# Kernel optimization log

Hardware: AMD Instinct MI355X
Metric: run time of the kernel (lower is better)

## Reference

```python
import jax, jax.numpy as jnp
import numpy as np

VOCAB, S, D, H, DH, L, W1S, DFF = 50265, 4096, 768, 12, 64, 2, 256, 3072


def layer_norm(x, g, b, eps=1e-5):
    m = jnp.mean(x, axis=-1, keepdims=True)
    v = jnp.mean((x - m) ** 2, axis=-1, keepdims=True)
    return (x - m) * jax.lax.rsqrt(v + eps) * g + b


def sliding_global_attn(q, k, v, att, w=W1S):
    # q,k,v: [B,H,S,Dh]; att: [B,S] float (1 real / 0 pad). Longformer-style
    # sliding window (one-sided w) + global attention on token 0.
    B, nh, S_, Dh = q.shape
    nc = S_ // w
    q = q * (Dh ** -0.5)
    k_pad = jnp.pad(k, ((0, 0), (0, 0), (w, w), (0, 0)))
    v_pad = jnp.pad(v, ((0, 0), (0, 0), (w, w), (0, 0)))
    idx = jnp.arange(nc)[:, None] * w + jnp.arange(3 * w)[None, :]  # [nc,3w] into padded axis
    k_band = k_pad[:, :, idx]  # [B,H,nc,3w,Dh]
    v_band = v_pad[:, :, idx]
    qc = q.reshape(B, nh, nc, w, Dh)
    s_loc = jnp.einsum('bhcqd,bhckd->bhcqk', qc, k_band)  # [B,H,nc,w,3w]
    rel = jnp.arange(3 * w)[None, :] - jnp.arange(w)[:, None]  # [w,3w]
    band_ok = (rel >= 0) & (rel <= 2 * w)
    key_abs = idx - w  # [nc,3w] absolute key positions
    in_seq = (key_abs >= 0) & (key_abs < S_) & (key_abs != 0)  # token 0 handled by global column
    key_real = att[:, jnp.clip(key_abs, 0, S_ - 1)] > 0  # [B,nc,3w]
    valid = band_ok[None, None, None] & in_seq[None, None, :, None, :] & key_real[:, None, :, None, :]
    s_loc = jnp.where(valid, s_loc, -1e9)
    s_g = jnp.einsum('bhcqd,bhd->bhcq', qc, k[:, :, 0])  # global key column
    p = jax.nn.softmax(jnp.concatenate([s_g[..., None], s_loc], axis=-1), axis=-1)
    out = (jnp.einsum('bhcq,bhd->bhcqd', p[..., 0], v[:, :, 0])
           + jnp.einsum('bhcqk,bhckd->bhcqd', p[..., 1:], v_band)).reshape(B, nh, S_, Dh)
    # global token 0 attends to everything
    s0 = jnp.where(att[:, None, :] > 0, jnp.einsum('bhd,bhsd->bhs', q[:, :, 0], k), -1e9)
    out0 = jnp.einsum('bhs,bhsd->bhd', jax.nn.softmax(s0, axis=-1), v)
    return out.at[:, :, 0].set(out0)


def setup_inputs() -> dict:
    key = jax.random.key(0)
    ks = jax.random.split(key, 16)
    sc = 0.02
    inp = {
        'input_ids': jax.random.randint(ks[0], (2, S), 0, VOCAB, dtype=jnp.int64)
        if jax.config.jax_enable_x64 else jax.random.randint(ks[0], (2, S), 0, VOCAB, dtype=jnp.int32),
        'attention_mask': jnp.ones((2, S), dtype=jnp.int32),
        'word_emb': sc * jax.random.normal(ks[1], (VOCAB, D), jnp.float32),
        'pos_emb': sc * jax.random.normal(ks[2], (S, D), jnp.float32),
        'emb_ln_g': jnp.ones((D,), jnp.float32), 'emb_ln_b': jnp.zeros((D,), jnp.float32),
        'Wq': sc * jax.random.normal(ks[3], (L, D, D), jnp.float32), 'bq': jnp.zeros((L, D), jnp.float32),
        'Wk': sc * jax.random.normal(ks[4], (L, D, D), jnp.float32), 'bk': jnp.zeros((L, D), jnp.float32),
        'Wv': sc * jax.random.normal(ks[5], (L, D, D), jnp.float32), 'bv': jnp.zeros((L, D), jnp.float32),
        'Wo': sc * jax.random.normal(ks[6], (L, D, D), jnp.float32), 'bo': jnp.zeros((L, D), jnp.float32),
        'ln1_g': jnp.ones((L, D), jnp.float32), 'ln1_b': jnp.zeros((L, D), jnp.float32),
        'Wf1': sc * jax.random.normal(ks[7], (L, D, DFF), jnp.float32), 'bf1': jnp.zeros((L, DFF), jnp.float32),
        'Wf2': sc * jax.random.normal(ks[8], (L, DFF, D), jnp.float32), 'bf2': jnp.zeros((L, D), jnp.float32),
        'ln2_g': jnp.ones((L, D), jnp.float32), 'ln2_b': jnp.zeros((L, D), jnp.float32),
        'Wh1': sc * jax.random.normal(ks[9], (D, 256), jnp.float32), 'bh1': jnp.zeros((256,), jnp.float32),
        'Wh2': sc * jax.random.normal(ks[10], (256, 14), jnp.float32), 'bh2': jnp.zeros((14,), jnp.float32),
    }
    return inp


def reference(input_ids, attention_mask, word_emb, pos_emb, emb_ln_g, emb_ln_b,
              Wq, bq, Wk, bk, Wv, bv, Wo, bo, ln1_g, ln1_b,
              Wf1, bf1, Wf2, bf2, ln2_g, ln2_b, Wh1, bh1, Wh2, bh2):
    B, S_ = input_ids.shape
    att = attention_mask.astype(jnp.float32)
    x = word_emb[input_ids] + pos_emb[None, :S_, :]
    x = layer_norm(x, emb_ln_g, emb_ln_b)
    for l in range(L):
        def heads(w, b):
            return (x @ w + b).reshape(B, S_, H, DH).transpose(0, 2, 1, 3)
        q = heads(Wq[l], bq[l]); k = heads(Wk[l], bk[l]); v = heads(Wv[l], bv[l])
        a = sliding_global_attn(q, k, v, att)
        a = a.transpose(0, 2, 1, 3).reshape(B, S_, D) @ Wo[l] + bo[l]
        x = layer_norm(x + a, ln1_g[l], ln1_b[l])
        f = jax.nn.gelu(x @ Wf1[l] + bf1[l]) @ Wf2[l] + bf2[l]
        x = layer_norm(x + f, ln2_g[l], ln2_b[l])
    # masked mean pool
    m = att[..., None]
    pooled = jnp.sum(x * m, axis=1) / jnp.clip(jnp.sum(m, axis=1), 1e-9)
    h = jax.nn.relu(pooled @ Wh1 + bh1)
    return jax.nn.sigmoid(h @ Wh2 + bh2) * 4.0
```

## Files before the change

### kernel.cpp

```cpp
#include <hip/hip_runtime.h>
#include <hip/hip_bf16.h>
#include <math.h>

#define S_LEN 4096
#define D_MODEL 768
#define NHEAD 12
#define DH 64
#define NLAYER 2
#define DFF 3072
#define BATCH 2
#define QSTR 2304

typedef __attribute__((ext_vector_type(8))) __bf16 bf16x8;
typedef __attribute__((ext_vector_type(4))) float f32x4;
typedef __attribute__((ext_vector_type(16))) float f32x16;

__device__ __forceinline__ unsigned short f2bf_bits(float f) {
  unsigned int u = __float_as_uint(f);
  unsigned int r = (u + 0x7fffu + ((u >> 16) & 1u)) >> 16;
  return (unsigned short)r;
}

__device__ __forceinline__ float bf2f(unsigned short u) {
  return __uint_as_float(((unsigned int)u) << 16);
}

__device__ __forceinline__ unsigned int cvtpk_bf16(float lo, float hi) {
  unsigned int d;
  asm("v_cvt_pk_bf16_f32 %0, %1, %2" : "=v"(d) : "v"(lo), "v"(hi));
  return d;
}

__device__ __forceinline__ float gelu_fast(float x) {
  float u = 0.7978845608028654f * (x + 0.044715f * x * x * x);
  float t2 = fminf(fmaxf(2.f * u, -18.f), 18.f);
  float e = __expf(t2);
  return 0.5f * x * (1.f + (e - 1.f) / (e + 1.f));
}

#define ASYNC_COPY16(gsrc, ldst)                                       \
  __builtin_amdgcn_global_load_lds(                                    \
      (const __attribute__((address_space(1))) void*)(gsrc),           \
      (__attribute__((address_space(3))) void*)(ldst), 16, 0, 0)

#define MFMA_BF16(a, b, c) __builtin_amdgcn_mfma_f32_16x16x32_bf16(a, b, c, 0, 0, 0)
#define MFMA32_BF16(a, b, c) __builtin_amdgcn_mfma_f32_32x32x16_bf16(a, b, c, 0, 0, 0)

__device__ __forceinline__ float blk_sum256(float v, float* lds) {
#pragma unroll
  for (int off = 32; off > 0; off >>= 1) v += __shfl_down(v, off, 64);
  __syncthreads();
  if ((threadIdx.x & 63) == 0) lds[threadIdx.x >> 6] = v;
  __syncthreads();
  return lds[0] + lds[1] + lds[2] + lds[3];
}

__global__ __launch_bounds__(256) void wconv_kernel(
    const float* __restrict__ Wq, const float* __restrict__ Wk,
    const float* __restrict__ Wv, const float* __restrict__ Wo,
    const float* __restrict__ Wf1, const float* __restrict__ Wf2,
    unsigned short* __restrict__ Wbf) {
  int id = blockIdx.x;
  const float* src;
  unsigned short* dst;
  int K, N, t;
  if (id < 4608) {
    int m = id / 576;
    t = id % 576;
    int layer = m >> 2, which = m & 3;
    const float* s = (which == 0) ? Wq : (which == 1) ? Wk : (which == 2) ? Wv : Wo;
    src = s + (size_t)layer * 589824;
    dst = Wbf + (size_t)layer * 7077888 + (size_t)which * 589824;
    K = 768; N = 768;
  } else if (id < 9216) {
    int j = id - 4608;
    int layer = j / 2304;
    t = j % 2304;
    src = Wf1 + (size_t)layer * 2359296;
    dst = Wbf + (size_t)layer * 7077888 + 2359296;
    K = 768; N = 3072;
  } else {
    int j = id - 9216;
    int layer = j / 2304;
    t = j % 2304;
    src = Wf2 + (size_t)layer * 2359296;
    dst = Wbf + (size_t)layer * 7077888 + 4718592;
    K = 3072; N = 768;
  }
  int tiles_n = N >> 5;
  int tk = t / tiles_n, tn = t % tiles_n;
  __shared__ float tile[32][33];
  int c = threadIdx.x & 31, r0 = threadIdx.x >> 5;
#pragma unroll
  for (int p = 0; p < 4; ++p) {
    int r = r0 + p * 8;
    tile[r][c] = src[(size_t)(tk * 32 + r) * N + tn * 32 + c];
  }
  __syncthreads();
#pragma unroll
  for (int p = 0; p < 4; ++p) {
    int r = r0 + p * 8;
    dst[(size_t)(tn * 32 + r) * K + tk * 32 + c] = f2bf_bits(tile[c][r]);
  }
}

__global__ __launch_bounds__(256) void embed_ln_kernel(
    const int* __restrict__ ids, const float* __restrict__ wemb,
    const float* __restrict__ pemb, const float* __restrict__ g,
    const float* __restrict__ b, unsigned short* __restrict__ Xb) {
  int row = blockIdx.x;
  int s = row % S_LEN;
  int id = ids[row];
  const float* we = wemb + (size_t)id * D_MODEL;
  const float* pe = pemb + (size_t)s * D_MODEL;
  int t = threadIdx.x;
  __shared__ float lds[4];
  float v0 = we[t] + pe[t];
  float v1 = we[t + 256] + pe[t + 256];
  float v2 = we[t + 512] + pe[t + 512];
  float mean = blk_sum256(v0 + v1 + v2, lds) * (1.f / 768.f);
  float d0 = v0 - mean, d1 = v1 - mean, d2 = v2 - mean;
  float var = blk_sum256(d0 * d0 + d1 * d1 + d2 * d2, lds) * (1.f / 768.f);
  float rs = rsqrtf(var + 1e-5f);
  unsigned short* xb = Xb + (size_t)row * D_MODEL;
  xb[t]       = f2bf_bits(d0 * rs * g[t] + b[t]);
  xb[t + 256] = f2bf_bits(d1 * rs * g[t + 256] + b[t + 256]);
  xb[t + 512] = f2bf_bits(d2 * rs * g[t + 512] + b[t + 512]);
}

__global__ __launch_bounds__(256) void ln_kernel(
    const float* __restrict__ T, const float* __restrict__ g,
    const float* __restrict__ b, unsigned short* __restrict__ Xb) {
  int row = blockIdx.x;
  const float* tp = T + (size_t)row * D_MODEL;
  int t = threadIdx.x;
  __shared__ float lds[4];
  float v0 = tp[t], v1 = tp[t + 256], v2 = tp[t + 512];
  float mean = blk_sum256(v0 + v1 + v2, lds) * (1.f / 768.f);
  float d0 = v0 - mean, d1 = v1 - mean, d2 = v2 - mean;
  float var = blk_sum256(d0 * d0 + d1 * d1 + d2 * d2, lds) * (1.f / 768.f);
  float rs = rsqrtf(var + 1e-5f);
  unsigned short* xb = Xb + (size_t)row * D_MODEL;
  xb[t]       = f2bf_bits(d0 * rs * g[t] + b[t]);
  xb[t + 256] = f2bf_bits(d1 * rs * g[t + 256] + b[t + 256]);
  xb[t + 512] = f2bf_bits(d2 * rs * g[t + 512] + b[t + 512]);
}

template <int MODE>
__global__ __launch_bounds__(256) void gemm32(
    const unsigned short* __restrict__ A, const unsigned short* __restrict__ Bt,
    const float* __restrict__ bias0, const float* __restrict__ bias1,
    const float* __restrict__ bias2, const unsigned short* __restrict__ ResBf,
    void* __restrict__ Cout, int M, int N, int K) {
  __shared__ unsigned short Abuf[3][128 * 32];
  __shared__ unsigned short Bbuf[3][128 * 32];
  const int tid = threadIdx.x;
  const int lane = tid & 63, w = tid >> 6;
  const int wm = w >> 1, wn = w & 1;
  const int l31 = lane & 31, l5 = lane >> 5;

  const int nbx = gridDim.x;
  const int nwg = nbx * gridDim.y;
  const int orig = blockIdx.y * nbx + blockIdx.x;
  const int wgid = (orig & 7) * (nwg >> 3) + (orig >> 3);
  const int m0 = (wgid / nbx) * 128, n0 = (wgid % nbx) * 128;

  f32x16 acc[2][2];
#pragma unroll
  for (int i = 0; i < 2; ++i)
#pragma unroll
    for (int j = 0; j < 2; ++j)
#pragma unroll
      for (int r = 0; r < 16; ++r) acc[i][j][r] = 0.f;

  const int s0 = w * 64 + lane, s1 = s0 + 256;
  const int r0 = s0 >> 2, c0 = (s0 & 3) ^ ((r0 >> 1) & 3);
  const int r1 = s1 >> 2, c1 = (s1 & 3) ^ ((r1 >> 1) & 3);
  const unsigned short* gA0 = A + (size_t)(m0 + r0) * K + c0 * 8;
  const unsigned short* gA1 = A + (size_t)(m0 + r1) * K + c1 * 8;
  const unsigned short* gB0 = Bt + (size_t)(n0 + r0) * K + c0 * 8;
  const unsigned short* gB1 = Bt + (size_t)(n0 + r1) * K + c1 * 8;
  const int dA0 = (w * 64) * 8, dA1 = (256 + w * 64) * 8;

  int aoff[2][2], boff[2][2];
#pragma unroll
  for (int mt = 0; mt < 2; ++mt) {
    int ra = wm * 64 + mt * 32 + l31;
    int rb = wn * 64 + mt * 32 + l31;
    int key_a = (ra >> 1) & 3, key_b = (rb >> 1) & 3;
#pragma unroll
    for (int ks = 0; ks < 2; ++ks) {
      aoff[mt][ks] = ra * 32 + ((((ks << 1) | l5) ^ key_a) << 3);
      boff[mt][ks] = rb * 32 + ((((ks << 1) | l5) ^ key_b) << 3);
    }
  }

#define STAGE(bsel)                                                       \
  {                                                                       \
    ASYNC_COPY16(gA0, &Abuf[bsel][dA0]);                                  \
    ASYNC_COPY16(gA1, &Abuf[bsel][dA1]);                                  \
    ASYNC_COPY16(gB0, &Bbuf[bsel][dA0]);                                  \
    ASYNC_COPY16(gB1, &Bbuf[bsel][dA1]);                                  \
    gA0 += 32; gA1 += 32; gB0 += 32; gB1 += 32;                           \
  }

  const int nk = K >> 5;
  STAGE(0);
  if (nk > 1) STAGE(1);
  asm volatile("s_waitcnt vmcnt(4)" ::: "memory");
  __builtin_amdgcn_s_barrier();
  __builtin_amdgcn_sched_barrier(0);

  int cur = 0;
  for (int kt = 0; kt < nk; ++kt) {
    if (kt + 2 < nk) {
      int nxt = cur + 2;
      if (nxt >= 3) nxt -= 3;
      STAGE(nxt);
    }
    bf16x8 av[2][2], bv[2][2];
#pragma unroll
    for (int mt = 0; mt < 2; ++mt)
#pragma unroll
      for (int ks = 0; ks < 2; ++ks) {
        av[mt][ks] = *(const bf16x8*)(&Abuf[cur][aoff[mt][ks]]);
        bv[mt][ks] = *(const bf16x8*)(&Bbuf[cur][boff[mt][ks]]);
      }
#pragma unroll
    for (int mt = 0; mt < 2; ++mt)
#pragma unroll
      for (int nt = 0; nt < 2; ++nt)
#pragma unroll
        for (int ks = 0; ks < 2; ++ks)
          acc[mt][nt] = MFMA32_BF16(av[mt][ks], bv[nt][ks], acc[mt][nt]);
    if (kt + 1 < nk) {
      if (kt + 2 < nk)
        asm volatile("s_waitcnt vmcnt(4)" ::: "memory");
      else
        asm volatile("s_waitcnt vmcnt(0)" ::: "memory");
      __builtin_amdgcn_s_barrier();
      __builtin_amdgcn_sched_barrier(0);
    }
    cur = (cur == 2) ? 0 : cur + 1;
  }
#undef STAGE

#pragma unroll
  for (int mt = 0; mt < 2; ++mt) {
#pragma unroll
    for (int nt = 0; nt < 2; ++nt) {
      int gc = n0 + wn * 64 + nt * 32 + l31;
      float bsv;
      if (MODE == 4)
        bsv = (gc < 768) ? bias0[gc] : (gc < 1536) ? bias1[gc - 768] : bias2[gc - 1536];
      else
        bsv = bias0[gc];
#pragma unroll
      for (int reg = 0; reg < 16; ++reg) {
        int gr = m0 + wm * 64 + mt * 32 + (reg & 3) + 8 * (reg >> 2) + 4 * l5;
        float v = acc[mt][nt][reg] + bsv;
        if (MODE == 1) v = gelu_fast(v);
        if (MODE == 4 && gc < 768) v *= 0.125f;
        if (MODE == 2) {
          v += bf2f(ResBf[(size_t)gr * 768 + gc]);
          ((float*)Cout)[(size_t)gr * N + gc] = v;
        } else {
          ((unsigned short*)Cout)[(size_t)gr * N + gc] = f2bf_bits(v);
        }
      }
    }
  }
}

__global__ __launch_bounds__(256) void vtrans_kernel(
    const unsigned short* __restrict__ Vsrc, unsigned short* __restrict__ Vt) {
  int kb = blockIdx.x, h = blockIdx.y, b = blockIdx.z;
  int k0 = kb * 64;
  const size_t bs = (size_t)b * S_LEN;
  const size_t bh = (size_t)(b * NHEAD + h);
  __shared__ unsigned short tile[64][72];
  int tid = threadIdx.x;
#pragma unroll
  for (int p = 0; p < 2; ++p) {
    int idx = p * 256 + tid;
    int key = idx >> 3, ch = idx & 7;
    bf16x8 v = *(const bf16x8*)(Vsrc + (bs + k0 + key) * QSTR + h * DH + ch * 8);
    *(bf16x8*)&tile[key][ch * 8] = v;
  }
  __syncthreads();
#pragma unroll
  for (int p = 0; p < 2; ++p) {
    int idx = p * 256 + tid;
    int d = idx >> 3, kc = idx & 7;
    unsigned int w0 = tile[kc * 8 + 0][d] | ((unsigned int)tile[kc * 8 + 1][d] << 16);
    unsigned int w1 = tile[kc * 8 + 2][d] | ((unsigned int)tile[kc * 8 + 3][d] << 16);
    unsigned int w2 = tile[kc * 8 + 4][d] | ((unsigned int)tile[kc * 8 + 5][d] << 16);
    unsigned int w3 = tile[kc * 8 + 6][d] | ((unsigned int)tile[kc * 8 + 7][d] << 16);
    uint4 out = make_uint4(w0, w1, w2, w3);
    *(uint4*)(Vt + (bh * 64 + d) * S_LEN + k0 + kc * 8) = out;
  }
}

__global__ __launch_bounds__(512) void band_attn_kernel(
    const unsigned short* __restrict__ Qg, const unsigned short* __restrict__ Kgb,
    const unsigned short* __restrict__ Vgb, const unsigned short* __restrict__ Vt,
    const int* __restrict__ att, unsigned short* __restrict__ Aout) {
  const int c = blockIdx.x, h = blockIdx.y, b = blockIdx.z;
  const int tid = threadIdx.x;
  const int lane = tid & 63, wq = tid >> 6;
  const int g = lane >> 4, cl = lane & 15;
  const size_t bs = (size_t)b * S_LEN;
  const size_t bh = (size_t)(b * NHEAD + h);

  __shared__ __align__(16) char smem[33280];

  if (c == 32) {
    float* sc = (float*)smem;
    float* q0 = sc + S_LEN;
    float* red = q0 + 64;
    float* part = red + 8;
    if (tid < 64) q0[tid] = bf2f(Qg[bs * QSTR + h * DH + tid]);
    __syncthreads();
    float lmax = -1e30f;
    for (int s = tid; s < S_LEN; s += 512) {
      const unsigned short* kp = Kgb + (bs + s) * QSTR + h * DH;
      float acc = 0.f;
#pragma unroll
      for (int cc = 0; cc < 8; ++cc) {
        uint4 u = *(const uint4*)(kp + cc * 8);
        const unsigned int* uu = (const unsigned int*)&u;
#pragma unroll
        for (int w2 = 0; w2 < 4; ++w2) {
          unsigned int x = uu[w2];
          acc += q0[cc * 8 + w2 * 2] * __uint_as_float(x << 16);
          acc += q0[cc * 8 + w2 * 2 + 1] * __uint_as_float(x & 0xffff0000u);
        }
      }
      acc = (att[b * S_LEN + s] > 0) ? acc : -1e9f;
      sc[s] = acc;
      lmax = fmaxf(lmax, acc);
    }
#pragma unroll
    for (int off = 32; off > 0; off >>= 1) lmax = fmaxf(lmax, __shfl_down(lmax, off, 64));
    __syncthreads();
    if (lane == 0) red[wq] = lmax;
    __syncthreads();
    float M = red[0];
#pragma unroll
    for (int i = 1; i < 8; ++i) M = fmaxf(M, red[i]);
    float lsum = 0.f;
    for (int s = tid; s < S_LEN; s += 512) {
      float p = __expf(sc[s] - M);
      sc[s] = p;
      lsum += p;
    }
#pragma unroll
    for (int off = 32; off > 0; off >>= 1) lsum += __shfl_down(lsum, off, 64);
    __syncthreads();
    if (lane == 0) red[wq] = lsum;
    __syncthreads();
    float L = red[0];
#pragma unroll
    for (int i = 1; i < 8; ++i) L += red[i];
    int d = tid & 63, chunk = tid >> 6;
    float acc2 = 0.f;
    for (int s = chunk * 512; s < (chunk + 1) * 512; ++s)
      acc2 += sc[s] * bf2f(Vgb[(bs + s) * QSTR + h * DH + d]);
    part[chunk * 64 + d] = acc2;
    __syncthreads();
    if (tid < 64) {
      float v = 0.f;
#pragma unroll
      for (int i = 0; i < 8; ++i) v += part[i * 64 + tid];
      Aout[bs * D_MODEL + h * DH + tid] = f2bf_bits(v / L);
    }
    return;
  }

  unsigned short* Klds = (unsigned short*)smem;
  unsigned short* Vlds = Klds + 2 * 4096;
  float* kmask = (float*)(Vlds + 2 * 4096);

  const int Q0 = c * 128;

  bf16x8 qf[2];
#pragma unroll
  for (int ks = 0; ks < 2; ++ks)
    qf[ks] = *(const bf16x8*)(Qg + (bs + Q0 + wq * 16 + cl) * QSTR +
                              h * DH + ks * 32 + g * 8);

  float mrun, lrun;
  f32x4 oacc[4];
  {
    float sg = 0.f;
#pragma unroll
    for (int ks = 0; ks < 2; ++ks) {
      bf16x8 k0 = *(const bf16x8*)(Kgb + bs * QSTR + h * DH + ks * 32 + g * 8);
#pragma unroll
      for (int j = 0; j < 8; ++j) sg += (float)qf[ks][j] * (float)k0[j];
    }
    sg += __shfl_xor(sg, 16, 64);
    sg += __shfl_xor(sg, 32, 64);
    mrun = sg;
    lrun = 1.f;
#pragma unroll
    for (int dt = 0; dt < 4; ++dt) {
      float v0d = bf2f(Vgb[bs * QSTR + h * DH + dt * 16 + cl]);
      oacc[dt] = (f32x4){v0d, v0d, v0d, v0d};
    }
  }

  const int jwlo = wq * 16, jwhi = wq * 16 + 543;
  const int tlo = (Q0 < 256) ? ((256 - Q0) >> 6) : 0;
  int thi = (S_LEN - Q0 + 256) >> 6;
  if (thi > 10) thi = 10;

  const int skey = tid >> 3, sch = tid & 7;
  const int swz = (sch ^ (skey & 7)) * 8;

  auto LOADT = [&](int t, bf16x8& kr, bf16x8& vr) {
    int kb0 = Q0 - 256 + t * 64;
    kr = *(const bf16x8*)(Kgb + (bs + kb0 + skey) * QSTR + h * DH + sch * 8);
    vr = *(const bf16x8*)(Vt + (bh * 64 + skey) * S_LEN + kb0 + sch * 8);
  };
  auto WRITET = [&](int p, int t, bf16x8 kr, bf16x8 vr) {
    *(bf16x8*)(Klds + p * 4096 + skey * 64 + swz) = kr;
    *(bf16x8*)(Vlds + p * 4096 + skey * 64 + swz) = vr;
    if (tid < 64) {
      int ka = Q0 - 256 + t * 64 + tid;
      kmask[p * 64 + tid] = (ka >= 1 && att[b * S_LEN + ka] > 0) ? 0.f : -1e9f;
    }
  };

  auto COMPUTE = [&](int p, int t) {
    if (t * 64 + 63 < jwlo || t * 64 > jwhi) return;
    f32x4 accs[4];
#pragma unroll
    for (int kt = 0; kt < 4; ++kt) accs[kt] = (f32x4){0.f, 0.f, 0.f, 0.f};
#pragma unroll
    for (int ks = 0; ks < 2; ++ks) {
      bf16x8 kf[4];
#pragma unroll
      for (int kt = 0; kt < 4; ++kt) {
        int key = kt * 16 + cl;
        kf[kt] = *(const bf16x8*)(Klds + p * 4096 + key * 64 +
                                  (((ks * 4 + g) ^ (key & 7)) * 8));
      }
#pragma unroll
      for (int kt = 0; kt < 4; ++kt)
        accs[kt] = MFMA_BF16(kf[kt], qf[ks], accs[kt]);
    }

    int iq = wq * 16 + cl;
    int relbase = t * 64 - iq;
    float pvv[4][4];
    float tmax = -1e30f;
#pragma unroll
    for (int kt = 0; kt < 4; ++kt)
#pragma unroll
      for (int r = 0; r < 4; ++r) {
        int key = kt * 16 + g * 4 + r;
        int rel = relbase + key;
        float x = accs[kt][r] + kmask[p * 64 + key];
        x = (rel >= 0 && rel <= 512) ? x : -1e9f;
        pvv[kt][r] = x;
        tmax = fmaxf(tmax, x);
      }
    tmax = fmaxf(tmax, __shfl_xor(tmax, 16, 64));
    tmax = fmaxf(tmax, __shfl_xor(tmax, 32, 64));
    float mnew = fmaxf(mrun, tmax);
    float scale = __expf(mrun - mnew);
    mrun = mnew;
    float psum = 0.f;
#pragma unroll
    for (int kt = 0; kt < 4; ++kt)
#pragma unroll
      for (int r = 0; r < 4; ++r) {
        float pp = __expf(pvv[kt][r] - mnew);
        pvv[kt][r] = pp;
        psum += pp;
      }
    psum += __shfl_xor(psum, 16, 64);
    psum += __shfl_xor(psum, 32, 64);
    lrun = lrun * scale + psum;
    float scr[4];
#pragma unroll
    for (int r = 0; r < 4; ++r) scr[r] = __shfl(scale, g * 4 + r, 64);
#pragma unroll
    for (int dt = 0; dt < 4; ++dt) {
      oacc[dt][0] *= scr[0];
      oacc[dt][1] *= scr[1];
      oacc[dt][2] *= scr[2];
      oacc[dt][3] *= scr[3];
    }
#pragma unroll
    for (int ks = 0; ks < 2; ++ks) {
      unsigned int E0D0 = cvtpk_bf16(pvv[ks * 2][0], pvv[ks * 2][1]);
      unsigned int E0D1 = cvtpk_bf16(pvv[ks * 2][2], pvv[ks * 2][3]);
      unsigned int E1D0 = cvtpk_bf16(pvv[ks * 2 + 1][0], pvv[ks * 2 + 1][1]);
      unsigned int E1D1 = cvtpk_bf16(pvv[ks * 2 + 1][2], pvv[ks * 2 + 1][3]);
      int src0 = ((lane >> 4) & 1) * 32 + cl;
      int src1 = src0 + 16;
      unsigned int a0 = (unsigned int)__shfl((int)E0D0, src0, 64);
      unsigned int a1 = (unsigned int)__shfl((int)E0D1, src0, 64);
      unsigned int a2 = (unsigned int)__shfl((int)E0D0, src1, 64);
      unsigned int a3 = (unsigned int)__shfl((int)E0D1, src1, 64);
      unsigned int b0 = (unsigned int)__shfl((int)E1D0, src0, 64);
      unsigned int b1 = (unsigned int)__shfl((int)E1D1, src0, 64);
      unsigned int b2 = (unsigned int)__shfl((int)E1D0, src1, 64);
      unsigned int b3 = (unsigned int)__shfl((int)E1D1, src1, 64);
      bool hi = lane >= 32;
      union { unsigned int u[4]; bf16x8 v; } af;
      af.u[0] = hi ? b0 : a0;
      af.u[1] = hi ? b1 : a1;
      af.u[2] = hi ? b2 : a2;
      af.u[3] = hi ? b3 : a3;
#pragma unroll
      for (int dt = 0; dt < 4; ++dt) {
        int d = dt * 16 + cl;
        bf16x8 vf = *(const bf16x8*)(Vlds + p * 4096 + d * 64 +
                                     (((ks * 4 + g) ^ (d & 7)) * 8));
        oacc[dt] = MFMA_BF16(af.v, vf, oacc[dt]);
      }
    }
  };

  bf16x8 kA, vA, kB, vB;
  LOADT(tlo, kA, vA);
  for (int t = tlo; t < thi; t += 2) {
    __builtin_amdgcn_s_barrier();
    WRITET(0, t, kA, vA);
    if (t + 1 < thi) LOADT(t + 1, kB, vB);
    asm volatile("s_waitcnt lgkmcnt(0)" ::: "memory");
    __builtin_amdgcn_s_barrier();
    __builtin_amdgcn_sched_barrier(0);
    COMPUTE(0, t);
    if (t + 1 >= thi) break;
    __builtin_amdgcn_s_barrier();
    WRITET(1, t + 1, kB, vB);
    if (t + 2 < thi) LOADT(t + 2, kA, vA);
    asm volatile("s_waitcnt lgkmcnt(0)" ::: "memory");
    __builtin_amdgcn_s_barrier();
    __builtin_amdgcn_sched_barrier(0);
    COMPUTE(1, t + 1);
  }

  float lr[4];
#pragma unroll
  for (int r = 0; r < 4; ++r) lr[r] = 1.f / __shfl(lrun, g * 4 + r, 64);
#pragma unroll
  for (int dt = 0; dt < 4; ++dt)
#pragma unroll
    for (int r = 0; r < 4; ++r) {
      int row = Q0 + wq * 16 + g * 4 + r;
      if (row != 0)
        Aout[(bs + row) * D_MODEL + h * DH + dt * 16 + cl] =
            f2bf_bits(oacc[dt][r] * lr[r]);
    }
}

__global__ __launch_bounds__(256) void pool1_kernel(
    const unsigned short* __restrict__ Xb, const int* __restrict__ att,
    float* __restrict__ ppart) {
  int sb = blockIdx.x, b = blockIdx.y, t = threadIdx.x;
  float a0 = 0.f, a1 = 0.f, a2 = 0.f;
  for (int s = sb * 256; s < sb * 256 + 256; ++s) {
    float a = (float)att[b * S_LEN + s];
    const unsigned short* xp = Xb + ((size_t)b * S_LEN + s) * D_MODEL;
    a0 += bf2f(xp[t]) * a; a1 += bf2f(xp[t + 256]) * a; a2 += bf2f(xp[t + 512]) * a;
  }
  float* pp = ppart + ((size_t)b * 16 + sb) * D_MODEL;
  pp[t] = a0; pp[t + 256] = a1; pp[t + 512] = a2;
}

__global__ __launch_bounds__(256) void pool2_kernel(
    const float* __restrict__ ppart, const int* __restrict__ att,
    float* __restrict__ pooled) {
  int b = blockIdx.x, t = threadIdx.x;
  float a0 = 0.f, a1 = 0.f, a2 = 0.f;
  for (int sb = 0; sb < 16; ++sb) {
    const float* pp = ppart + ((size_t)b * 16 + sb) * D_MODEL;
    a0 += pp[t]; a1 += pp[t + 256]; a2 += pp[t + 512];
  }
  float cnt = 0.f;
  for (int s = 0; s < S_LEN; ++s) cnt += (float)att[b * S_LEN + s];
  cnt = fmaxf(cnt, 1e-9f);
  pooled[b * D_MODEL + t]       = a0 / cnt;
  pooled[b * D_MODEL + t + 256] = a1 / cnt;
  pooled[b * D_MODEL + t + 512] = a2 / cnt;
}

__global__ __launch_bounds__(256) void head_kernel(
    const float* __restrict__ pooled, const float* __restrict__ Wh1,
    const float* __restrict__ bh1, const float* __restrict__ Wh2,
    const float* __restrict__ bh2, float* __restrict__ out) {
  __shared__ float hbuf[2][256];
  int t = threadIdx.x;
  for (int b = 0; b < 2; ++b) {
    float acc = bh1[t];
    for (int d = 0; d < D_MODEL; ++d) acc += pooled[b * D_MODEL + d] * Wh1[d * 256 + t];
    hbuf[b][t] = fmaxf(acc, 0.f);
  }
  __syncthreads();
  if (t < 28) {
    int b = t / 14, j = t % 14;
    float acc = bh2[j];
    for (int i = 0; i < 256; ++i) acc += hbuf[b][i] * Wh2[i * 14 + j];
    out[t] = 4.f / (1.f + __expf(-acc));
  }
}

extern "C" void kernel_launch(void* const* d_in, const int* in_sizes, int n_in,
                              void* d_out, int out_size, void* d_ws,
                              size_t ws_size, hipStream_t stream) {
  const int* ids    = (const int*)d_in[0];
  const int* att    = (const int*)d_in[1];
  const float* wemb = (const float*)d_in[2];
  const float* pemb = (const float*)d_in[3];
  const float* elng = (const float*)d_in[4];
  const float* elnb = (const float*)d_in[5];
  const float* Wq   = (const float*)d_in[6];
  const float* bq   = (const float*)d_in[7];
  const float* Wk   = (const float*)d_in[8];
  const float* bk   = (const float*)d_in[9];
  const float* Wv   = (const float*)d_in[10];
  const float* bv   = (const float*)d_in[11];
  const float* Wo   = (const float*)d_in[12];
  const float* bo   = (const float*)d_in[13];
  const float* ln1g = (const float*)d_in[14];
  const float* ln1b = (const float*)d_in[15];
  const float* Wf1  = (const float*)d_in[16];
  const float* bf1  = (const float*)d_in[17];
  const float* Wf2  = (const float*)d_in[18];
  const float* bf2  = (const float*)d_in[19];
  const float* ln2g = (const float*)d_in[20];
  const float* ln2b = (const float*)d_in[21];
  const float* Wh1  = (const float*)d_in[22];
  const float* bh1  = (const float*)d_in[23];
  const float* Wh2  = (const float*)d_in[24];
  const float* bh2  = (const float*)d_in[25];

  const int M = BATCH * S_LEN;
  float* ws = (float*)d_ws;
  float* T = ws;
  unsigned short* QKV  = (unsigned short*)(ws + 6291456);
  unsigned short* Vt   = (unsigned short*)(ws + 11010048);
  unsigned short* Abbf = (unsigned short*)(ws + 12582912);
  unsigned short* Xbf  = (unsigned short*)(ws + 15728640);
  unsigned short* FFbf = (unsigned short*)(ws + 18874368);
  unsigned short* Wbf  = (unsigned short*)(ws + 31457280);
  float* pooled = ws + 38535168;
  float* ppart  = ws + 38536704;

  wconv_kernel<<<13824, 256, 0, stream>>>(Wq, Wk, Wv, Wo, Wf1, Wf2, Wbf);
  embed_ln_kernel<<<M, 256, 0, stream>>>(ids, wemb, pemb, elng, elnb, Xbf);

  for (int l = 0; l < NLAYER; ++l) {
    const unsigned short* wqkv = Wbf + (size_t)l * 7077888;
    const unsigned short* wot  = wqkv + 1769472;
    const unsigned short* wf1t = wqkv + 2359296;
    const unsigned short* wf2t = wqkv + 4718592;

    gemm32<4><<<dim3(18, 64), 256, 0, stream>>>(
        Xbf, wqkv, bq + l * D_MODEL, bk + l * D_MODEL, bv + l * D_MODEL,
        nullptr, QKV, M, QSTR, 768);

    vtrans_kernel<<<dim3(64, NHEAD, BATCH), 256, 0, stream>>>(QKV + 1536, Vt);
    band_attn_kernel<<<dim3(33, NHEAD, BATCH), 512, 0, stream>>>(
        QKV, QKV + 768, QKV + 1536, Vt, att, Abbf);

    gemm32<2><<<dim3(6, 64), 256, 0, stream>>>(
        Abbf, wot, bo + l * D_MODEL, nullptr, nullptr, Xbf, T, M, 768, 768);
    ln_kernel<<<M, 256, 0, stream>>>(T, ln1g + l * D_MODEL, ln1b + l * D_MODEL, Xbf);

    gemm32<1><<<dim3(24, 64), 256, 0, stream>>>(
        Xbf, wf1t, bf1 + l * DFF, nullptr, nullptr, nullptr, FFbf, M, DFF, 768);
    gemm32<2><<<dim3(6, 64), 256, 0, stream>>>(
        FFbf, wf2t, bf2 + l * D_MODEL, nullptr, nullptr, Xbf, T, M, 768, DFF);
    ln_kernel<<<M, 256, 0, stream>>>(T, ln2g + l * D_MODEL, ln2b + l * D_MODEL, Xbf);
  }

  pool1_kernel<<<dim3(16, BATCH), 256, 0, stream>>>(Xbf, att, ppart);
  pool2_kernel<<<BATCH, 256, 0, stream>>>(ppart, att, pooled);
  head_kernel<<<1, 256, 0, stream>>>(pooled, Wh1, bh1, Wh2, bh2, (float*)d_out);
}
```

Measured before the change: 998.3 us.

## Restructure band attention: 256-query tiles, async triple-buffered K/V, XCD-aware block mapping

```diff
diff --git a/kernel.cpp b/kernel.cpp
--- a/kernel.cpp
+++ b/kernel.cpp
@@ -305,16 +305,17 @@
     const unsigned short* __restrict__ Qg, const unsigned short* __restrict__ Kgb,
     const unsigned short* __restrict__ Vgb, const unsigned short* __restrict__ Vt,
     const int* __restrict__ att, unsigned short* __restrict__ Aout) {
-  const int c = blockIdx.x, h = blockIdx.y, b = blockIdx.z;
+  const int bid = blockIdx.x;
   const int tid = threadIdx.x;
   const int lane = tid & 63, wq = tid >> 6;
   const int g = lane >> 4, cl = lane & 15;
-  const size_t bs = (size_t)b * S_LEN;
-  const size_t bh = (size_t)(b * NHEAD + h);
-
-  __shared__ __align__(16) char smem[33280];
-
-  if (c == 32) {
+
+  __shared__ __align__(16) char smem[52224];
+
+  if (bid >= 384) {
+    int g2 = bid - 384;
+    int h = g2 % NHEAD, b = g2 / NHEAD;
+    const size_t bs = (size_t)b * S_LEN;
     float* sc = (float*)smem;
     float* q0 = sc + S_LEN;
     float* red = q0 + 64;
@@ -377,66 +378,83 @@
     return;
   }
 
+  const int xcd = bid & 7, within = bid >> 3;
+  const int flat = xcd * 48 + within;
+  const int c = flat & 15;
+  const int hb = flat >> 4;
+  const int h = hb % NHEAD, b = hb / NHEAD;
+  const size_t bs = (size_t)b * S_LEN;
+  const size_t bh = (size_t)(b * NHEAD + h);
+
   unsigned short* Klds = (unsigned short*)smem;
-  unsigned short* Vlds = Klds + 2 * 4096;
-  float* kmask = (float*)(Vlds + 2 * 4096);
-
-  const int Q0 = c * 128;
-
-  bf16x8 qf[2];
-#pragma unroll
-  for (int ks = 0; ks < 2; ++ks)
-    qf[ks] = *(const bf16x8*)(Qg + (bs + Q0 + wq * 16 + cl) * QSTR +
-                              h * DH + ks * 32 + g * 8);
-
-  float mrun, lrun;
-  f32x4 oacc[4];
-  {
+  unsigned short* Vlds = Klds + 3 * 4096;
+  float* kmaskAll = (float*)(Vlds + 3 * 4096);
+
+  const int Q0 = c * 256;
+
+  bf16x8 qf[2][2];
+#pragma unroll
+  for (int qt = 0; qt < 2; ++qt)
+#pragma unroll
+    for (int ks = 0; ks < 2; ++ks)
+      qf[qt][ks] = *(const bf16x8*)(Qg + (bs + Q0 + wq * 32 + qt * 16 + cl) * QSTR +
+                                    h * DH + ks * 32 + g * 8);
+
+  float mrun[2], lrun[2];
+  f32x4 oacc[2][4];
+#pragma unroll
+  for (int qt = 0; qt < 2; ++qt) {
     float sg = 0.f;
 #pragma unroll
     for (int ks = 0; ks < 2; ++ks) {
       bf16x8 k0 = *(const bf16x8*)(Kgb + bs * QSTR + h * DH + ks * 32 + g * 8);
 #pragma unroll
-      for (int j = 0; j < 8; ++j) sg += (float)qf[ks][j] * (float)k0[j];
+      for (int j = 0; j < 8; ++j) sg += (float)qf[qt][ks][j] * (float)k0[j];
     }
     sg += __shfl_xor(sg, 16, 64);
     sg += __shfl_xor(sg, 32, 64);
-    mrun = sg;
-    lrun = 1.f;
-#pragma unroll
-    for (int dt = 0; dt < 4; ++dt) {
-      float v0d = bf2f(Vgb[bs * QSTR + h * DH + dt * 16 + cl]);
-      oacc[dt] = (f32x4){v0d, v0d, v0d, v0d};
-    }
-  }
-
-  const int jwlo = wq * 16, jwhi = wq * 16 + 543;
-  const int tlo = (Q0 < 256) ? ((256 - Q0) >> 6) : 0;
-  int thi = (S_LEN - Q0 + 256) >> 6;
-  if (thi > 10) thi = 10;
+    mrun[qt] = sg;
+    lrun[qt] = 1.f;
+  }
+#pragma unroll
+  for (int dt = 0; dt < 4; ++dt) {
+    float v0d = bf2f(Vgb[bs * QSTR + h * DH + dt * 16 + cl]);
+    f32x4 vv = {v0d, v0d, v0d, v0d};
+    oacc[0][dt] = vv;
+    oacc[1][dt] = vv;
+  }
+  for (int i = tid; i < 768; i += 512) {
+    int ka = Q0 - 256 + i;
+    kmaskAll[i] = (ka >= 1 && ka < S_LEN && att[b * S_LEN + ka] > 0) ? 0.f : -1e9f;
+  }
+  __syncthreads();
+
+  const int jlo = wq * 32, jhi = wq * 32 + 543;
+  const int tlo = (Q0 < 256) ? 4 : 0;
+  int thi = (S_LEN + 256 - Q0) >> 6;
+  if (thi > 12) thi = 12;
 
   const int skey = tid >> 3, sch = tid & 7;
-  const int swz = (sch ^ (skey & 7)) * 8;
-
-  auto LOADT = [&](int t, bf16x8& kr, bf16x8& vr) {
+  const int srcswzK = (sch ^ (skey & 7)) * 8;
+
+  auto STAGE_T = [&](int t) {
+    int p = t % 3;
     int kb0 = Q0 - 256 + t * 64;
-    kr = *(const bf16x8*)(Kgb + (bs + kb0 + skey) * QSTR + h * DH + sch * 8);
-    vr = *(const bf16x8*)(Vt + (bh * 64 + skey) * S_LEN + kb0 + sch * 8);
+    const unsigned short* srcK = Kgb + (bs + kb0 + skey) * QSTR + h * DH + srcswzK;
+    const unsigned short* srcV = Vt + (bh * 64 + skey) * S_LEN + kb0 + srcswzK;
+    ASYNC_COPY16(srcK, Klds + p * 4096 + wq * 512);
+    ASYNC_COPY16(srcV, Vlds + p * 4096 + wq * 512);
   };
-  auto WRITET = [&](int p, int t, bf16x8 kr, bf16x8 vr) {
-    *(bf16x8*)(Klds + p * 4096 + skey * 64 + swz) = kr;
-    *(bf16x8*)(Vlds + p * 4096 + skey * 64 + swz) = vr;
-    if (tid < 64) {
-      int ka = Q0 - 256 + t * 64 + tid;
-      kmask[p * 64 + tid] = (ka >= 1 && att[b * S_LEN + ka] > 0) ? 0.f : -1e9f;
-    }
-  };
-
-  auto COMPUTE = [&](int p, int t) {
-    if (t * 64 + 63 < jwlo || t * 64 > jwhi) return;
-    f32x4 accs[4];
-#pragma unroll
-    for (int kt = 0; kt < 4; ++kt) accs[kt] = (f32x4){0.f, 0.f, 0.f, 0.f};
+
+  auto COMPUTE = [&](int t) {
+    if (t * 64 + 63 < jlo || t * 64 > jhi) return;
+    int p = t % 3;
+    f32x4 accs[4][2];
+#pragma unroll
+    for (int kt = 0; kt < 4; ++kt) {
+      accs[kt][0] = (f32x4){0.f, 0.f, 0.f, 0.f};
+      accs[kt][1] = (f32x4){0.f, 0.f, 0.f, 0.f};
+    }
 #pragma unroll
     for (int ks = 0; ks < 2; ++ks) {
       bf16x8 kf[4];
@@ -447,116 +465,117 @@
                                   (((ks * 4 + g) ^ (key & 7)) * 8));
       }
 #pragma unroll
+      for (int kt = 0; kt < 4; ++kt) {
+        accs[kt][0] = MFMA_BF16(kf[kt], qf[0][ks], accs[kt][0]);
+        accs[kt][1] = MFMA_BF16(kf[kt], qf[1][ks], accs[kt][1]);
+      }
+    }
+
+#pragma unroll
+    for (int qt = 0; qt < 2; ++qt) {
+      int iq = wq * 32 + qt * 16 + cl;
+      int relbase = t * 64 - iq;
+      float pvv[4][4];
+      float tmax = -1e30f;
+#pragma unroll
       for (int kt = 0; kt < 4; ++kt)
-        accs[kt] = MFMA_BF16(kf[kt], qf[ks], accs[kt]);
-    }
-
-    int iq = wq * 16 + cl;
-    int relbase = t * 64 - iq;
-    float pvv[4][4];
-    float tmax = -1e30f;
-#pragma unroll
-    for (int kt = 0; kt < 4; ++kt)
-#pragma unroll
-      for (int r = 0; r < 4; ++r) {
-        int key = kt * 16 + g * 4 + r;
-        int rel = relbase + key;
-        float x = accs[kt][r] + kmask[p * 64 + key];
-        x = (rel >= 0 && rel <= 512) ? x : -1e9f;
-        pvv[kt][r] = x;
-        tmax = fmaxf(tmax, x);
+#pragma unroll
+        for (int r = 0; r < 4; ++r) {
+          int key = kt * 16 + g * 4 + r;
+          int rel = relbase + key;
+          float x = accs[kt][qt][r] + kmaskAll[t * 64 + key];
+          x = (rel >= 0 && rel <= 512) ? x : -1e9f;
+          pvv[kt][r] = x;
+          tmax = fmaxf(tmax, x);
+        }
+      tmax = fmaxf(tmax, __shfl_xor(tmax, 16, 64));
+      tmax = fmaxf(tmax, __shfl_xor(tmax, 32, 64));
+      float mnew = fmaxf(mrun[qt], tmax);
+      float scale = __expf(mrun[qt] - mnew);
+      mrun[qt] = mnew;
+      float psum = 0.f;
+#pragma unroll
+      for (int kt = 0; kt < 4; ++kt)
+#pragma unroll
+        for (int r = 0; r < 4; ++r) {
+          float pp = __expf(pvv[kt][r] - mnew);
+          pvv[kt][r] = pp;
+          psum += pp;
+        }
+      psum += __shfl_xor(psum, 16, 64);
+      psum += __shfl_xor(psum, 32, 64);
+      lrun[qt] = lrun[qt] * scale + psum;
+      float scr[4];
+#pragma unroll
+      for (int r = 0; r < 4; ++r) scr[r] = __shfl(scale, g * 4 + r, 64);
+#pragma unroll
+      for (int dt = 0; dt < 4; ++dt) {
+        oacc[qt][dt][0] *= scr[0];
+        oacc[qt][dt][1] *= scr[1];
+        oacc[qt][dt][2] *= scr[2];
+        oacc[qt][dt][3] *= scr[3];
       }
-    tmax = fmaxf(tmax, __shfl_xor(tmax, 16, 64));
-    tmax = fmaxf(tmax, __shfl_xor(tmax, 32, 64));
-    float mnew = fmaxf(mrun, tmax);
-    float scale = __expf(mrun - mnew);
-    mrun = mnew;
-    float psum = 0.f;
-#pragma unroll
-    for (int kt = 0; kt < 4; ++kt)
-#pragma unroll
-      for (int r = 0; r < 4; ++r) {
-        float pp = __expf(pvv[kt][r] - mnew);
-        pvv[kt][r] = pp;
-        psum += pp;
+#pragma unroll
+      for (int ks = 0; ks < 2; ++ks) {
+        unsigned int E0D0 = cvtpk_bf16(pvv[ks * 2][0], pvv[ks * 2][1]);
+        unsigned int E0D1 = cvtpk_bf16(pvv[ks * 2][2], pvv[ks * 2][3]);
+        unsigned int E1D0 = cvtpk_bf16(pvv[ks * 2 + 1][0], pvv[ks * 2 + 1][1]);
+        unsigned int E1D1 = cvtpk_bf16(pvv[ks * 2 + 1][2], pvv[ks * 2 + 1][3]);
+        int src0 = ((lane >> 4) & 1) * 32 + cl;
+        int src1 = src0 + 16;
+        unsigned int a0 = (unsigned int)__shfl((int)E0D0, src0, 64);
+        unsigned int a1 = (unsigned int)__shfl((int)E0D1, src0, 64);
+        unsigned int a2 = (unsigned int)__shfl((int)E0D0, src1, 64);
+        unsigned int a3 = (unsigned int)__shfl((int)E0D1, src1, 64);
+        unsigned int b0 = (unsigned int)__shfl((int)E1D0, src0, 64);
+        unsigned int b1 = (unsigned int)__shfl((int)E1D1, src0, 64);
+        unsigned int b2 = (unsigned int)__shfl((int)E1D0, src1, 64);
+        unsigned int b3 = (unsigned int)__shfl((int)E1D1, src1, 64);
+        bool hi = lane >= 32;
+        union { unsigned int u[4]; bf16x8 v; } af;
+        af.u[0] = hi ? b0 : a0;
+        af.u[1] = hi ? b1 : a1;
+        af.u[2] = hi ? b2 : a2;
+        af.u[3] = hi ? b3 : a3;
+#pragma unroll
+        for (int dt = 0; dt < 4; ++dt) {
+          int d = dt * 16 + cl;
+          bf16x8 vf = *(const bf16x8*)(Vlds + p * 4096 + d * 64 +
+                                       (((ks * 4 + g) ^ (d & 7)) * 8));
+          oacc[qt][dt] = MFMA_BF16(af.v, vf, oacc[qt][dt]);
+        }
       }
-    psum += __shfl_xor(psum, 16, 64);
-    psum += __shfl_xor(psum, 32, 64);
-    lrun = lrun * scale + psum;
-    float scr[4];
-#pragma unroll
-    for (int r = 0; r < 4; ++r) scr[r] = __shfl(scale, g * 4 + r, 64);
-#pragma unroll
-    for (int dt = 0; dt < 4; ++dt) {
-      oacc[dt][0] *= scr[0];
-      oacc[dt][1] *= scr[1];
-      oacc[dt][2] *= scr[2];
-      oacc[dt][3] *= scr[3];
-    }
-#pragma unroll
-    for (int ks = 0; ks < 2; ++ks) {
-      unsigned int E0D0 = cvtpk_bf16(pvv[ks * 2][0], pvv[ks * 2][1]);
-      unsigned int E0D1 = cvtpk_bf16(pvv[ks * 2][2], pvv[ks * 2][3]);
-      unsigned int E1D0 = cvtpk_bf16(pvv[ks * 2 + 1][0], pvv[ks * 2 + 1][1]);
-      unsigned int E1D1 = cvtpk_bf16(pvv[ks * 2 + 1][2], pvv[ks * 2 + 1][3]);
-      int src0 = ((lane >> 4) & 1) * 32 + cl;
-      int src1 = src0 + 16;
-      unsigned int a0 = (unsigned int)__shfl((int)E0D0, src0, 64);
-      unsigned int a1 = (unsigned int)__shfl((int)E0D1, src0, 64);
-      unsigned int a2 = (unsigned int)__shfl((int)E0D0, src1, 64);
-      unsigned int a3 = (unsigned int)__shfl((int)E0D1, src1, 64);
-      unsigned int b0 = (unsigned int)__shfl((int)E1D0, src0, 64);
-      unsigned int b1 = (unsigned int)__shfl((int)E1D1, src0, 64);
-      unsigned int b2 = (unsigned int)__shfl((int)E1D0, src1, 64);
-      unsigned int b3 = (unsigned int)__shfl((int)E1D1, src1, 64);
-      bool hi = lane >= 32;
-      union { unsigned int u[4]; bf16x8 v; } af;
-      af.u[0] = hi ? b0 : a0;
-      af.u[1] = hi ? b1 : a1;
-      af.u[2] = hi ? b2 : a2;
-      af.u[3] = hi ? b3 : a3;
-#pragma unroll
-      for (int dt = 0; dt < 4; ++dt) {
-        int d = dt * 16 + cl;
-        bf16x8 vf = *(const bf16x8*)(Vlds + p * 4096 + d * 64 +
-                                     (((ks * 4 + g) ^ (d & 7)) * 8));
-        oacc[dt] = MFMA_BF16(af.v, vf, oacc[dt]);
-      }
     }
   };
 
-  bf16x8 kA, vA, kB, vB;
-  LOADT(tlo, kA, vA);
-  for (int t = tlo; t < thi; t += 2) {
-    __builtin_amdgcn_s_barrier();
-    WRITET(0, t, kA, vA);
-    if (t + 1 < thi) LOADT(t + 1, kB, vB);
-    asm volatile("s_waitcnt lgkmcnt(0)" ::: "memory");
+  STAGE_T(tlo);
+  if (tlo + 1 < thi) STAGE_T(tlo + 1);
+  for (int t = tlo; t < thi; ++t) {
+    if (t + 1 < thi)
+      asm volatile("s_waitcnt vmcnt(2)" ::: "memory");
+    else
+      asm volatile("s_waitcnt vmcnt(0)" ::: "memory");
     __builtin_amdgcn_s_barrier();
     __builtin_amdgcn_sched_barrier(0);
-    COMPUTE(0, t);
-    if (t + 1 >= thi) break;
-    __builtin_amdgcn_s_barrier();
-    WRITET(1, t + 1, kB, vB);
-    if (t + 2 < thi) LOADT(t + 2, kA, vA);
-    asm volatile("s_waitcnt lgkmcnt(0)" ::: "memory");
-    __builtin_amdgcn_s_barrier();
-    __builtin_amdgcn_sched_barrier(0);
-    COMPUTE(1, t + 1);
-  }
-
-  float lr[4];
-#pragma unroll
-  for (int r = 0; r < 4; ++r) lr[r] = 1.f / __shfl(lrun, g * 4 + r, 64);
-#pragma unroll
-  for (int dt = 0; dt < 4; ++dt)
-#pragma unroll
-    for (int r = 0; r < 4; ++r) {
-      int row = Q0 + wq * 16 + g * 4 + r;
-      if (row != 0)
-        Aout[(bs + row) * D_MODEL + h * DH + dt * 16 + cl] =
-            f2bf_bits(oacc[dt][r] * lr[r]);
-    }
+    if (t + 2 < thi) STAGE_T(t + 2);
+    COMPUTE(t);
+  }
+
+#pragma unroll
+  for (int qt = 0; qt < 2; ++qt) {
+    float lr[4];
+#pragma unroll
+    for (int r = 0; r < 4; ++r) lr[r] = 1.f / __shfl(lrun[qt], g * 4 + r, 64);
+#pragma unroll
+    for (int dt = 0; dt < 4; ++dt)
+#pragma unroll
+      for (int r = 0; r < 4; ++r) {
+        int row = Q0 + wq * 32 + qt * 16 + g * 4 + r;
+        if (row != 0)
+          Aout[(bs + row) * D_MODEL + h * DH + dt * 16 + cl] =
+              f2bf_bits(oacc[qt][dt][r] * lr[r]);
+      }
+  }
 }
 
 __global__ __launch_bounds__(256) void pool1_kernel(
@@ -666,7 +685,7 @@
         nullptr, QKV, M, QSTR, 768);
 
     vtrans_kernel<<<dim3(64, NHEAD, BATCH), 256, 0, stream>>>(QKV + 1536, Vt);
-    band_attn_kernel<<<dim3(33, NHEAD, BATCH), 512, 0, stream>>>(
+    band_attn_kernel<<<408, 512, 0, stream>>>(
         QKV, QKV + 768, QKV + 1536, Vt, att, Abbf);
 
     gemm32<2><<<dim3(6, 64), 256, 0, stream>>>(
```

Result: faster. 831.3 us (-16.7%).
